# Kernel tuning notes

Measured on AMD Instinct MI355X. Metric: run time of the kernel, lower is better.

The kernel has to match this reference:

```python
import jax, jax.numpy as jnp
import numpy as np

B, S, D, U = 32, 4096, 512, 128

def setup_inputs() -> dict:
    key = jax.random.key(0)
    k1, k2, k3, k4, k5 = jax.random.split(key, 5)
    query = jax.random.normal(k1, (B, D), dtype=jnp.float32)
    values = jax.random.normal(k2, (B, S, D), dtype=jnp.float32)
    s = 1.0 / np.sqrt(D)
    W1 = jax.random.normal(k3, (D, U), dtype=jnp.float32) * s
    W2 = jax.random.normal(k4, (D, U), dtype=jnp.float32) * s
    V = jax.random.normal(k5, (U, 1), dtype=jnp.float32) * (1.0 / np.sqrt(U))
    b1 = jnp.zeros((U,), dtype=jnp.float32)
    b2 = jnp.zeros((U,), dtype=jnp.float32)
    bv = jnp.zeros((1,), dtype=jnp.float32)
    return {"query": query, "values": values, "W1": W1, "b1": b1,
            "W2": W2, "b2": b2, "V": V, "bv": bv}

def reference(query, values, W1, b1, W2, b2, V, bv):
    # query: [B, D] -> [B, 1, U]; values: [B, S, D] -> [B, S, U]
    q_proj = (query @ W1 + b1)[:, None, :]                  # [B, 1, U]
    v_proj = jnp.einsum('bsd,du->bsu', values, W2) + b2      # [B, S, U]
    score = jnp.tanh(q_proj + v_proj) @ V + bv               # [B, S, 1]
    attention_weights = jax.nn.softmax(score, axis=1)        # [B, S, 1]
    context_vector = jnp.sum(attention_weights * values, axis=1)  # [B, D]
    return context_vector, attention_weights
```

## Files before the change

### kernel.cpp

```cpp
#include <hip/hip_runtime.h>
#include <math.h>

#define NB 32
#define NS 4096
#define ND 512
#define NU 128
#define RR 64

typedef __bf16 bf16x8 __attribute__((ext_vector_type(8)));
typedef unsigned short u16x8 __attribute__((ext_vector_type(8)));
typedef float f32x4 __attribute__((ext_vector_type(4)));

union FragCvt { u16x8 u; bf16x8 b; };

__device__ inline unsigned short f2bf(float x) {
  union { float f; unsigned u; } v; v.f = x;
  return (unsigned short)((v.u + 0x7FFFu + ((v.u >> 16) & 1u)) >> 16);
}
__device__ inline float bf2f(unsigned int bits16) {
  union { unsigned u; float f; } v; v.u = bits16 << 16;
  return v.f;
}
__device__ inline float fast_tanh(float x) {
  x = fminf(9.f, fmaxf(-9.f, x));
  float e2 = __expf(2.f * x);
  return (e2 - 1.f) * __builtin_amdgcn_rcpf(e2 + 1.f);
}
__device__ inline int bswz(int byte) { return byte ^ (((byte >> 7) & 7) << 4); }
__device__ inline int aswz(int row, int byte) { return row * 1024 + (byte ^ ((row & 7) << 4)); }

__global__ void prep_qb(const float* __restrict__ q, const float* __restrict__ W1,
                        const float* __restrict__ b1, const float* __restrict__ b2,
                        float* __restrict__ qb) {
  const int bb = blockIdx.x >> 4;
  const int kc = blockIdx.x & 15;
  const int u  = threadIdx.x & 127;
  const int dh = threadIdx.x >> 7;
  const int d0 = kc * 32 + dh * 16;
  const float* qr = q + bb * ND + d0;
  const float* w  = W1 + (size_t)d0 * NU + u;
  float s = (kc == 0 && dh == 0) ? (b1[u] + b2[u]) : 0.f;
  #pragma unroll
  for (int j = 0; j < 16; ++j) s += qr[j] * w[j * NU];
  atomicAdd(qb + bb * NU + u, s);
}

__global__ void prep_w2s(const float* __restrict__ W2, unsigned short* __restrict__ w2s) {
  const int idx = blockIdx.x * 256 + threadIdx.x;
  const int u = idx & 127;
  const int r = idx >> 7;
  const int k = r & 31, kt = r >> 5;
  w2s[kt * 4096 + u * 32 + k] = f2bf(W2[(size_t)(kt * 32 + k) * NU + u]);
}

__global__ __launch_bounds__(256, 2) void fused_attn(
    const float* __restrict__ values,
    const float* __restrict__ qb,
    const unsigned short* __restrict__ w2s,
    const float* __restrict__ V,
    const float* __restrict__ bvp,
    float* __restrict__ wout,
    float* __restrict__ Cacc,
    float* __restrict__ Lacc)
{
  __shared__ unsigned short Alds[RR * 512];
  __shared__ union {
    unsigned short B[2][4096];
    struct { float sw[64]; float e[64]; } t;
  } Bsh;

  const int tid = threadIdx.x;
  const int b = blockIdx.x >> 6;
  const int chunk = blockIdx.x & 63;
  const int s0 = chunk * RR;

  const uint4* w2s4 = (const uint4*)w2s;
  uint4 breg0 = w2s4[tid * 2];
  uint4 breg1 = w2s4[tid * 2 + 1];

  const float* vbase = values + ((size_t)b * NS + s0) * ND;
  char* Ab = (char*)Alds;
  #pragma unroll
  for (int ii = 0; ii < 32; ii += 8) {
    float4 v[8];
    #pragma unroll
    for (int j = 0; j < 8; ++j) {
      const int f = tid + 256 * (ii + j);
      v[j] = *(const float4*)(vbase + (f >> 7) * ND + (f & 127) * 4);
    }
    #pragma unroll
    for (int j = 0; j < 8; ++j) {
      const int f = tid + 256 * (ii + j);
      const int row = f >> 7, c4 = f & 127;
      ushort4 pk;
      pk.x = f2bf(v[j].x); pk.y = f2bf(v[j].y); pk.z = f2bf(v[j].z); pk.w = f2bf(v[j].w);
      *(ushort4*)(Ab + aswz(row, c4 * 8)) = pk;
    }
  }

  const int wave = tid >> 6, lane = tid & 63;
  const int quad = lane >> 4, lidx = lane & 15;

  f32x4 acc[8] = {{0.f,0.f,0.f,0.f},{0.f,0.f,0.f,0.f},{0.f,0.f,0.f,0.f},{0.f,0.f,0.f,0.f},
                  {0.f,0.f,0.f,0.f},{0.f,0.f,0.f,0.f},{0.f,0.f,0.f,0.f},{0.f,0.f,0.f,0.f}};
  const int arow = wave * 16 + lidx;
  const int arswz = (arow & 7) << 4;
  const char* Arow = Ab + arow * 1024;

  for (int kt = 0; kt < 16; ++kt) {
    char* bdst = (char*)Bsh.B[kt & 1];
    const int by0 = tid * 32;
    *(uint4*)(bdst + bswz(by0))      = breg0;
    *(uint4*)(bdst + bswz(by0 + 16)) = breg1;
    __syncthreads();
    if (kt < 15) {
      breg0 = w2s4[(kt + 1) * 512 + tid * 2];
      breg1 = w2s4[(kt + 1) * 512 + tid * 2 + 1];
    }
    FragCvt af; af.u = *(const u16x8*)(Arow + ((kt * 64 + quad * 16) ^ arswz));
    const char* bsrc = (const char*)Bsh.B[kt & 1];
    #pragma unroll
    for (int nt = 0; nt < 8; ++nt) {
      const int bb2 = (nt * 16 + lidx) * 64 + quad * 16;
      FragCvt bf; bf.u = *(const u16x8*)(bsrc + bswz(bb2));
      acc[nt] = __builtin_amdgcn_mfma_f32_16x16x32_bf16(af.b, bf.b, acc[nt], 0, 0, 0);
    }
  }

  float part[4] = {0.f, 0.f, 0.f, 0.f};
  #pragma unroll
  for (int nt = 0; nt < 8; ++nt) {
    const int col = nt * 16 + lidx;
    const float qv = qb[b * NU + col];
    const float vv = V[col];
    #pragma unroll
    for (int r = 0; r < 4; ++r)
      part[r] += fast_tanh(acc[nt][r] + qv) * vv;
  }
  #pragma unroll
  for (int m = 1; m <= 8; m <<= 1) {
    #pragma unroll
    for (int r = 0; r < 4; ++r) part[r] += __shfl_xor(part[r], m, 64);
  }
  if (lidx == 0) {
    #pragma unroll
    for (int r = 0; r < 4; ++r) Bsh.t.sw[wave * 16 + quad * 4 + r] = part[r];
  }
  __syncthreads();

  if (tid < 64) {
    float s = Bsh.t.sw[tid];
    float e = __expf(s + *bvp);
    wout[(size_t)b * NS + s0 + tid] = e;
    Bsh.t.e[tid] = e;
    float es = e;
    #pragma unroll
    for (int m = 1; m <= 32; m <<= 1) es += __shfl_xor(es, m, 64);
    if (tid == 0) atomicAdd(Lacc + b, es);
  }
  __syncthreads();

  const int d0b = tid * 4;
  float c0 = 0.f, c1 = 0.f;
  #pragma unroll 8
  for (int r = 0; r < RR; ++r) {
    const float w = Bsh.t.e[r];
    const unsigned int pk = *(const unsigned int*)(Ab + aswz(r, d0b));
    c0 += w * bf2f(pk & 0xFFFFu);
    c1 += w * bf2f(pk >> 16);
  }
  const int d0 = tid * 2;
  atomicAdd(Cacc + b * ND + d0, c0);
  atomicAdd(Cacc + b * ND + d0 + 1, c1);
}

__global__ void finalize(const float* __restrict__ Cacc, const float* __restrict__ Lacc,
                         float* __restrict__ out) {
  int idx = blockIdx.x * 256 + threadIdx.x;
  if (idx < NB * ND) {
    int b = idx >> 9;
    out[idx] = Cacc[idx] / Lacc[b];
  } else {
    int j = idx - NB * ND;
    int b = j >> 12;
    out[idx] = out[idx] / Lacc[b];
  }
}

extern "C" void kernel_launch(void* const* d_in, const int* in_sizes, int n_in,
                              void* d_out, int out_size, void* d_ws, size_t ws_size,
                              hipStream_t stream) {
  const float* query  = (const float*)d_in[0];
  const float* values = (const float*)d_in[1];
  const float* W1     = (const float*)d_in[2];
  const float* b1     = (const float*)d_in[3];
  const float* W2     = (const float*)d_in[4];
  const float* b2     = (const float*)d_in[5];
  const float* V      = (const float*)d_in[6];
  const float* bv     = (const float*)d_in[7];
  float* out = (float*)d_out;

  char* ws = (char*)d_ws;
  float* Cacc = (float*)ws;
  float* Lacc = (float*)(ws + 65536);
  float* qb   = (float*)(ws + 66048);
  unsigned short* w2s = (unsigned short*)(ws + 66048 + 16384);

  hipMemsetAsync(ws, 0, 66048 + 16384, stream);

  prep_qb <<<NB * 16, 256, 0, stream>>>(query, W1, b1, b2, qb);
  prep_w2s<<<256, 256, 0, stream>>>(W2, w2s);
  fused_attn<<<NB * (NS / RR), 256, 0, stream>>>(values, qb, w2s, V, bv,
                                                 out + NB * ND, Cacc, Lacc);
  finalize<<<(NB * ND + NB * NS) / 256, 256, 0, stream>>>(Cacc, Lacc, out);
}
```

Before: 416.0 us.

## Keep full W2 in LDS and stream values directly into register MFMA fragments

The fused kernel now loads all of bf16 W2 (128 KB) into shared memory once per block and uses 512 persistent-style blocks of 512 threads, each covering two 128-row chunks. Values rows are loaded straight from global into per-lane bf16 A-fragments held in registers, so the LDS staging of values and the per-k-tile B double-buffer syncs go away. The context accumulation reuses those register fragments through a butterfly shuffle reduction instead of re-reading LDS. This trades heavy register pressure (16 fragments plus 64-float reduction arrays) and one block per CU for less LDS traffic and fewer barriers, and it adds many more shuffles and uncoalesced-ish strided global loads.

```diff
diff --git a/kernel.cpp b/kernel.cpp
--- a/kernel.cpp
+++ b/kernel.cpp
@@ -5,7 +5,6 @@
 #define NS 4096
 #define ND 512
 #define NU 128
-#define RR 64
 
 typedef __bf16 bf16x8 __attribute__((ext_vector_type(8)));
 typedef unsigned short u16x8 __attribute__((ext_vector_type(8)));
@@ -27,7 +26,6 @@
   return (e2 - 1.f) * __builtin_amdgcn_rcpf(e2 + 1.f);
 }
 __device__ inline int bswz(int byte) { return byte ^ (((byte >> 7) & 7) << 4); }
-__device__ inline int aswz(int row, int byte) { return row * 1024 + (byte ^ ((row & 7) << 4)); }
 
 __global__ void prep_qb(const float* __restrict__ q, const float* __restrict__ W1,
                         const float* __restrict__ b1, const float* __restrict__ b2,
@@ -53,7 +51,7 @@
   w2s[kt * 4096 + u * 32 + k] = f2bf(W2[(size_t)(kt * 32 + k) * NU + u]);
 }
 
-__global__ __launch_bounds__(256, 2) void fused_attn(
+__global__ __launch_bounds__(512, 1) void fused_attn(
     const float* __restrict__ values,
     const float* __restrict__ qb,
     const unsigned short* __restrict__ w2s,
@@ -63,115 +61,128 @@
     float* __restrict__ Cacc,
     float* __restrict__ Lacc)
 {
-  __shared__ unsigned short Alds[RR * 512];
-  __shared__ union {
-    unsigned short B[2][4096];
-    struct { float sw[64]; float e[64]; } t;
-  } Bsh;
+  __shared__ unsigned short Bs[16 * 4096];
 
   const int tid = threadIdx.x;
-  const int b = blockIdx.x >> 6;
-  const int chunk = blockIdx.x & 63;
-  const int s0 = chunk * RR;
+  const int blk = blockIdx.x;
+  const int b = blk >> 4;
+  const int pair = blk & 15;
 
   const uint4* w2s4 = (const uint4*)w2s;
-  uint4 breg0 = w2s4[tid * 2];
-  uint4 breg1 = w2s4[tid * 2 + 1];
-
-  const float* vbase = values + ((size_t)b * NS + s0) * ND;
-  char* Ab = (char*)Alds;
-  #pragma unroll
-  for (int ii = 0; ii < 32; ii += 8) {
-    float4 v[8];
-    #pragma unroll
-    for (int j = 0; j < 8; ++j) {
-      const int f = tid + 256 * (ii + j);
-      v[j] = *(const float4*)(vbase + (f >> 7) * ND + (f & 127) * 4);
-    }
-    #pragma unroll
-    for (int j = 0; j < 8; ++j) {
-      const int f = tid + 256 * (ii + j);
-      const int row = f >> 7, c4 = f & 127;
-      ushort4 pk;
-      pk.x = f2bf(v[j].x); pk.y = f2bf(v[j].y); pk.z = f2bf(v[j].z); pk.w = f2bf(v[j].w);
-      *(ushort4*)(Ab + aswz(row, c4 * 8)) = pk;
-    }
-  }
+  #pragma unroll
+  for (int i = 0; i < 16; ++i) {
+    const int m = i * 512 + tid;
+    const uint4 v = w2s4[m];
+    *(uint4*)((char*)Bs + (m >> 9) * 8192 + bswz((m & 511) * 16)) = v;
+  }
+  __syncthreads();
 
   const int wave = tid >> 6, lane = tid & 63;
   const int quad = lane >> 4, lidx = lane & 15;
 
-  f32x4 acc[8] = {{0.f,0.f,0.f,0.f},{0.f,0.f,0.f,0.f},{0.f,0.f,0.f,0.f},{0.f,0.f,0.f,0.f},
-                  {0.f,0.f,0.f,0.f},{0.f,0.f,0.f,0.f},{0.f,0.f,0.f,0.f},{0.f,0.f,0.f,0.f}};
-  const int arow = wave * 16 + lidx;
-  const int arswz = (arow & 7) << 4;
-  const char* Arow = Ab + arow * 1024;
-
-  for (int kt = 0; kt < 16; ++kt) {
-    char* bdst = (char*)Bsh.B[kt & 1];
-    const int by0 = tid * 32;
-    *(uint4*)(bdst + bswz(by0))      = breg0;
-    *(uint4*)(bdst + bswz(by0 + 16)) = breg1;
-    __syncthreads();
-    if (kt < 15) {
-      breg0 = w2s4[(kt + 1) * 512 + tid * 2];
-      breg1 = w2s4[(kt + 1) * 512 + tid * 2 + 1];
-    }
-    FragCvt af; af.u = *(const u16x8*)(Arow + ((kt * 64 + quad * 16) ^ arswz));
-    const char* bsrc = (const char*)Bsh.B[kt & 1];
+  int boff[8];
+  #pragma unroll
+  for (int nt = 0; nt < 8; ++nt)
+    boff[nt] = bswz((nt * 16 + lidx) * 64 + quad * 16);
+
+  float qv[8], vv[8];
+  #pragma unroll
+  for (int nt = 0; nt < 8; ++nt) {
+    qv[nt] = qb[b * NU + nt * 16 + lidx];
+    vv[nt] = V[nt * 16 + lidx];
+  }
+  const float bv = *bvp;
+
+  for (int c = 0; c < 2; ++c) {
+    const int s0c = (pair * 2 + c) * 128;
+    const int row = s0c + wave * 16 + lidx;
+    const float* abase = values + ((size_t)b * NS + row) * ND + quad * 8;
+
+    f32x4 acc[8] = {{0.f,0.f,0.f,0.f},{0.f,0.f,0.f,0.f},{0.f,0.f,0.f,0.f},{0.f,0.f,0.f,0.f},
+                    {0.f,0.f,0.f,0.f},{0.f,0.f,0.f,0.f},{0.f,0.f,0.f,0.f},{0.f,0.f,0.f,0.f}};
+    FragCvt a[16];
+    #pragma unroll
+    for (int kt = 0; kt < 16; ++kt) {
+      const float4 a0 = *(const float4*)(abase + kt * 32);
+      const float4 a1 = *(const float4*)(abase + kt * 32 + 4);
+      a[kt].b[0] = (__bf16)a0.x; a[kt].b[1] = (__bf16)a0.y;
+      a[kt].b[2] = (__bf16)a0.z; a[kt].b[3] = (__bf16)a0.w;
+      a[kt].b[4] = (__bf16)a1.x; a[kt].b[5] = (__bf16)a1.y;
+      a[kt].b[6] = (__bf16)a1.z; a[kt].b[7] = (__bf16)a1.w;
+      const char* bt = (const char*)Bs + kt * 8192;
+      #pragma unroll
+      for (int nt = 0; nt < 8; ++nt) {
+        FragCvt bf; bf.u = *(const u16x8*)(bt + boff[nt]);
+        acc[nt] = __builtin_amdgcn_mfma_f32_16x16x32_bf16(a[kt].b, bf.b, acc[nt], 0, 0, 0);
+      }
+    }
+
+    float part[4] = {0.f, 0.f, 0.f, 0.f};
     #pragma unroll
     for (int nt = 0; nt < 8; ++nt) {
-      const int bb2 = (nt * 16 + lidx) * 64 + quad * 16;
-      FragCvt bf; bf.u = *(const u16x8*)(bsrc + bswz(bb2));
-      acc[nt] = __builtin_amdgcn_mfma_f32_16x16x32_bf16(af.b, bf.b, acc[nt], 0, 0, 0);
-    }
-  }
-
-  float part[4] = {0.f, 0.f, 0.f, 0.f};
-  #pragma unroll
-  for (int nt = 0; nt < 8; ++nt) {
-    const int col = nt * 16 + lidx;
-    const float qv = qb[b * NU + col];
-    const float vv = V[col];
-    #pragma unroll
-    for (int r = 0; r < 4; ++r)
-      part[r] += fast_tanh(acc[nt][r] + qv) * vv;
-  }
-  #pragma unroll
-  for (int m = 1; m <= 8; m <<= 1) {
-    #pragma unroll
-    for (int r = 0; r < 4; ++r) part[r] += __shfl_xor(part[r], m, 64);
-  }
-  if (lidx == 0) {
-    #pragma unroll
-    for (int r = 0; r < 4; ++r) Bsh.t.sw[wave * 16 + quad * 4 + r] = part[r];
-  }
-  __syncthreads();
-
-  if (tid < 64) {
-    float s = Bsh.t.sw[tid];
-    float e = __expf(s + *bvp);
-    wout[(size_t)b * NS + s0 + tid] = e;
-    Bsh.t.e[tid] = e;
+      #pragma unroll
+      for (int r = 0; r < 4; ++r)
+        part[r] += fast_tanh(acc[nt][r] + qv[nt]) * vv[nt];
+    }
+    #pragma unroll
+    for (int m = 1; m <= 8; m <<= 1) {
+      #pragma unroll
+      for (int r = 0; r < 4; ++r) part[r] += __shfl_xor(part[r], m, 64);
+    }
+    const int r3 = lidx & 3;
+    float tmp = (r3 == 0) ? part[0] : (r3 == 1) ? part[1] : (r3 == 2) ? part[2] : part[3];
+    const float sc = __shfl(tmp, (lidx >> 2) * 16 + lidx, 64);
+    const float e = __expf(sc + bv);
+    if (quad == 0) wout[(size_t)b * NS + s0c + wave * 16 + lidx] = e;
     float es = e;
-    #pragma unroll
-    for (int m = 1; m <= 32; m <<= 1) es += __shfl_xor(es, m, 64);
-    if (tid == 0) atomicAdd(Lacc + b, es);
-  }
-  __syncthreads();
-
-  const int d0b = tid * 4;
-  float c0 = 0.f, c1 = 0.f;
-  #pragma unroll 8
-  for (int r = 0; r < RR; ++r) {
-    const float w = Bsh.t.e[r];
-    const unsigned int pk = *(const unsigned int*)(Ab + aswz(r, d0b));
-    c0 += w * bf2f(pk & 0xFFFFu);
-    c1 += w * bf2f(pk >> 16);
-  }
-  const int d0 = tid * 2;
-  atomicAdd(Cacc + b * ND + d0, c0);
-  atomicAdd(Cacc + b * ND + d0 + 1, c1);
+    es += __shfl_xor(es, 1, 64); es += __shfl_xor(es, 2, 64);
+    es += __shfl_xor(es, 4, 64); es += __shfl_xor(es, 8, 64);
+    if (lane == 0) atomicAdd(Lacc + b, es);
+
+    const bool h0 = lidx & 1, h1 = lidx & 2, h2 = lidx & 4, h3 = lidx & 8;
+    float cA[8][8];
+    #pragma unroll
+    for (int k = 0; k < 8; ++k) {
+      #pragma unroll
+      for (int j = 0; j < 8; ++j) {
+        const float lo = e * bf2f(a[2 * k].u[j]);
+        const float hi = e * bf2f(a[2 * k + 1].u[j]);
+        const float mine = h0 ? hi : lo;
+        const float oth  = h0 ? lo : hi;
+        cA[k][j] = mine + __shfl_xor(oth, 1, 64);
+      }
+    }
+    float cB[4][8];
+    #pragma unroll
+    for (int k = 0; k < 4; ++k) {
+      #pragma unroll
+      for (int j = 0; j < 8; ++j) {
+        const float mine = h1 ? cA[2 * k + 1][j] : cA[2 * k][j];
+        const float oth  = h1 ? cA[2 * k][j] : cA[2 * k + 1][j];
+        cB[k][j] = mine + __shfl_xor(oth, 2, 64);
+      }
+    }
+    float cC[2][8];
+    #pragma unroll
+    for (int k = 0; k < 2; ++k) {
+      #pragma unroll
+      for (int j = 0; j < 8; ++j) {
+        const float mine = h2 ? cB[2 * k + 1][j] : cB[2 * k][j];
+        const float oth  = h2 ? cB[2 * k][j] : cB[2 * k + 1][j];
+        cC[k][j] = mine + __shfl_xor(oth, 4, 64);
+      }
+    }
+    float cD[8];
+    #pragma unroll
+    for (int j = 0; j < 8; ++j) {
+      const float mine = h3 ? cC[1][j] : cC[0][j];
+      const float oth  = h3 ? cC[0][j] : cC[1][j];
+      cD[j] = mine + __shfl_xor(oth, 8, 64);
+    }
+    #pragma unroll
+    for (int j = 0; j < 8; ++j)
+      atomicAdd(Cacc + b * ND + lidx * 32 + quad * 8 + j, cD[j]);
+  }
 }
 
 __global__ void finalize(const float* __restrict__ Cacc, const float* __restrict__ Lacc,
@@ -210,7 +221,7 @@
 
   prep_qb <<<NB * 16, 256, 0, stream>>>(query, W1, b1, b2, qb);
   prep_w2s<<<256, 256, 0, stream>>>(W2, w2s);
-  fused_attn<<<NB * (NS / RR), 256, 0, stream>>>(values, qb, w2s, V, bv,
-                                                 out + NB * ND, Cacc, Lacc);
+  fused_attn<<<512, 512, 0, stream>>>(values, qb, w2s, V, bv,
+                                      out + NB * ND, Cacc, Lacc);
   finalize<<<(NB * ND + NB * NS) / 256, 256, 0, stream>>>(Cacc, Lacc, out);
 }
```

New measurement: 808.3 us. +94.3%, slower.
